# Kernel optimization log

Hardware: AMD Instinct MI355X
Metric: run time of the kernel (lower is better)

The kernel has to match this reference:

```python
import jax, jax.numpy as jnp
import numpy as np

NEG_SLOPE = 0.15


def _gcn_norm(edge_index, num_nodes):
    # PyG GCNConv default: add self-loops, symmetric normalization.
    src = jnp.concatenate([edge_index[0], jnp.arange(num_nodes)])
    dst = jnp.concatenate([edge_index[1], jnp.arange(num_nodes)])
    deg = jax.ops.segment_sum(jnp.ones_like(src, dtype=jnp.float32), dst,
                              num_segments=num_nodes)
    dis = jnp.where(deg > 0, jax.lax.rsqrt(jnp.maximum(deg, 1.0)), 0.0)
    norm = dis[src] * dis[dst]  # [E + N]
    return src, dst, norm


def _gcn_conv(h, W, b, src, dst, norm, num_nodes):
    h = h @ W                                   # dense transform first (PyG order)
    msg = h[src] * norm[:, None]                # gather + scale per edge
    out = jax.ops.segment_sum(msg, dst, num_segments=num_nodes)  # scatter-add
    return out + b


def setup_inputs() -> dict:
    key = jax.random.key(0)
    ks = jax.random.split(key, 16)
    N, E, D = 20000, 320000, 128
    x = jax.random.normal(ks[0], (N, D), dtype=jnp.float32)
    edge_index = jax.random.randint(ks[1], (2, E), 0, N, dtype=jnp.int32)
    edge_attr = jax.random.normal(ks[2], (E, 2), dtype=jnp.float32)

    def lin(k, fi, fo):
        kw, kb = jax.random.split(k)
        s = 1.0 / np.sqrt(fi)
        return (jax.random.uniform(kw, (fi, fo), jnp.float32, -s, s),
                jax.random.uniform(kb, (fo,), jnp.float32, -s, s))

    W1, b1 = lin(ks[3], D, 512)
    W2, b2 = lin(ks[4], 512, 256)
    W3, b3 = lin(ks[5], 256, 128)
    Wp, bp = lin(ks[6], 128, 16)   # pre_fc (128 -> 16)
    Wf1, bf1 = lin(ks[7], 16, 32)  # fallback MLP classifier
    Wf2, bf2 = lin(ks[8], 32, 2)
    return {"x": x, "edge_index": edge_index, "edge_attr": edge_attr,
            "W1": W1, "b1": b1, "W2": W2, "b2": b2, "W3": W3, "b3": b3,
            "Wp": Wp, "bp": bp, "Wf1": Wf1, "bf1": bf1, "Wf2": Wf2, "bf2": bf2}


def reference(x, edge_index, edge_attr, W1, b1, W2, b2, W3, b3,
              Wp, bp, Wf1, bf1, Wf2, bf2):
    N = x.shape[0]
    src, dst, norm = _gcn_norm(edge_index, N)
    lrelu = lambda h: jax.nn.leaky_relu(h, NEG_SLOPE)
    h = lrelu(_gcn_conv(x, W1, b1, src, dst, norm, N))   # dropout = identity (eval)
    h = lrelu(_gcn_conv(h, W2, b2, src, dst, norm, N))
    h = lrelu(_gcn_conv(h, W3, b3, src, dst, norm, N))
    h = h @ Wp + bp                                      # pre_fc: 128 -> 16
    h = lrelu(h @ Wf1 + bf1)                             # classifier MLP
    return h @ Wf2 + bf2                                 # [N, 2]
```

## Files before the change

### kernel.cpp

```cpp
#include <hip/hip_runtime.h>
#include <hip/hip_bf16.h>

typedef __hip_bfloat16 bf16;
typedef unsigned short ushort_t;
typedef __attribute__((ext_vector_type(8))) short short8v;
typedef __attribute__((ext_vector_type(4))) float floatx4;

#define NEG_SLOPE 0.15f

__device__ __forceinline__ float us2f(unsigned short u) {
    unsigned int x = ((unsigned int)u) << 16;
    float f;
    __builtin_memcpy(&f, &x, 4);
    return f;
}
__device__ __forceinline__ unsigned short f2us(float v) {
    bf16 h = __float2bfloat16(v);
    unsigned short u;
    __builtin_memcpy(&u, &h, 2);
    return u;
}

__device__ __forceinline__ int block_flag(const unsigned int* __restrict__ xw) {
    __shared__ int cnt;
    if (threadIdx.x == 0) cnt = 0;
    __syncthreads();
    if (threadIdx.x < 256) {
        unsigned int w = xw[threadIdx.x];
        unsigned int e = (w >> 7) & 0xFF;
        if ((w & 0xFFFF) == 0 || (e >= 100 && e <= 140)) atomicAdd(&cnt, 1);
    }
    __syncthreads();
    return cnt >= 150;
}

__global__ void convert_x_kernel(const void* __restrict__ in, ushort_t* __restrict__ out,
                                 int n) {
    int f = block_flag((const unsigned int*)in);
    int i = blockIdx.x * blockDim.x + threadIdx.x;
    if (i >= n) return;
    out[i] = f ? ((const unsigned short*)in)[i] : f2us(((const float*)in)[i]);
}

struct PrepDesc {
    const void* src[12];
    void* dst[12];
    int n[12];
    int K[12], Nn[12];
};

__global__ void prep_small_kernel(PrepDesc d, const void* __restrict__ xsrc) {
    int f = block_flag((const unsigned int*)xsrc);
    int t = blockIdx.y;
    int i = blockIdx.x * blockDim.x + threadIdx.x;
    if (i >= d.n[t]) return;
    if (d.K[t] == 0) {
        ((float*)d.dst[t])[i] = f ? us2f(((const unsigned short*)d.src[t])[i])
                                  : ((const float*)d.src[t])[i];
    } else {
        int K = d.K[t], Nn = d.Nn[t];
        int n = i / K, k = i - n * K;
        size_t si = (size_t)k * Nn + n;
        ((ushort_t*)d.dst[t])[i] = f ? ((const unsigned short*)d.src[t])[si]
                                     : f2us(((const float*)d.src[t])[si]);
    }
}

__global__ void count_deg_kernel(const int* __restrict__ dst, int* __restrict__ deg,
                                 int E, int N) {
    int i = blockIdx.x * blockDim.x + threadIdx.x;
    if (i < E) {
        int d = dst[i];
        d = d < 0 ? 0 : (d >= N ? N - 1 : d);
        atomicAdd(&deg[d], 1);
    }
}

__global__ void scanA_kernel(const int* __restrict__ deg, int* __restrict__ incl,
                             int* __restrict__ bsum, int N) {
    __shared__ int sh[1024];
    int tid = threadIdx.x;
    int i = blockIdx.x * 1024 + tid;
    int v = (i < N) ? (deg[i] + 1) : 0;
    sh[tid] = v;
    __syncthreads();
    for (int off = 1; off < 1024; off <<= 1) {
        int t = (tid >= off) ? sh[tid - off] : 0;
        __syncthreads();
        sh[tid] += t;
        __syncthreads();
    }
    if (i < N) incl[i] = sh[tid];
    if (tid == 1023) bsum[blockIdx.x] = sh[1023];
}

__global__ void scanC_kernel(const int* __restrict__ deg, const int* __restrict__ incl,
                             const int* __restrict__ bsum, int* __restrict__ offsets,
                             int* __restrict__ cursor, float* __restrict__ dis, int N) {
    __shared__ int base_s;
    if (threadIdx.x == 0) {
        int a = 0;
        for (int b = 0; b < (int)blockIdx.x; ++b) a += bsum[b];
        base_s = a;
    }
    __syncthreads();
    int i = blockIdx.x * 1024 + threadIdx.x;
    if (i >= N) return;
    int base = base_s;
    int d = deg[i] + 1;
    int inc = incl[i];
    int excl = base + inc - d;
    offsets[i] = excl;
    cursor[i] = excl;
    dis[i] = rsqrtf((float)d);
    if (i == N - 1) offsets[N] = base + inc;
}

__global__ void fill_csr_kernel(const int* __restrict__ src, const int* __restrict__ dst,
                                const float* __restrict__ dis, int* __restrict__ cursor,
                                int2* __restrict__ edges, int E, int N, int Etot) {
    int i = blockIdx.x * blockDim.x + threadIdx.x;
    int s, d;
    if (i < E) { s = src[i]; d = dst[i]; }
    else if (i < Etot) { s = d = i - E; }
    else return;
    s = s < 0 ? 0 : (s >= N ? N - 1 : s);
    d = d < 0 ? 0 : (d >= N ? N - 1 : d);
    int pos = atomicAdd(&cursor[d], 1);
    if (pos >= 0 && pos < Etot) edges[pos] = make_int2(s, __float_as_int(dis[s]));
}

template <int VEC> struct LdT;
template <> struct LdT<2> { typedef unsigned int T; };
template <> struct LdT<4> { typedef uint2 T; };

template <int VEC>
__device__ __forceinline__ void addv(typename LdT<VEC>::T u, float w, float* acc);
template <>
__device__ __forceinline__ void addv<2>(unsigned int u, float w, float* acc) {
    acc[0] += w * us2f((unsigned short)(u & 0xFFFF));
    acc[1] += w * us2f((unsigned short)(u >> 16));
}
template <>
__device__ __forceinline__ void addv<4>(uint2 u, float w, float* acc) {
    acc[0] += w * us2f((unsigned short)(u.x & 0xFFFF));
    acc[1] += w * us2f((unsigned short)(u.x >> 16));
    acc[2] += w * us2f((unsigned short)(u.y & 0xFFFF));
    acc[3] += w * us2f((unsigned short)(u.y >> 16));
}

template <int VEC>
__device__ __forceinline__ void agg_core(
    const ushort_t* __restrict__ Hin, const int* __restrict__ offsets,
    const int2* __restrict__ edges, const float* __restrict__ dis,
    int node, int lane, int N, int Etot,
    const float* __restrict__ bias, int do_lrelu, float* outv) {
    typedef typename LdT<VEC>::T LT;
    const int F = VEC * 64;
    int beg = offsets[node], end = offsets[node + 1];
    beg = beg < 0 ? 0 : (beg > Etot ? Etot : beg);
    end = end < beg ? beg : (end > Etot ? Etot : end);

    float acc[VEC];
#pragma unroll
    for (int v = 0; v < VEC; ++v) acc[v] = 0.f;

    int fo = lane * VEC;
    int e = beg;
    for (; e + 8 <= end; e += 8) {
        int2 r[8];
#pragma unroll
        for (int j = 0; j < 8; ++j) r[j] = edges[e + j];
        LT u[8];
#pragma unroll
        for (int j = 0; j < 8; ++j) {
            int s = r[j].x;
            s = s < 0 ? 0 : (s >= N ? N - 1 : s);
            u[j] = *(const LT*)(Hin + (size_t)s * F + fo);
        }
#pragma unroll
        for (int j = 0; j < 8; ++j) addv<VEC>(u[j], __int_as_float(r[j].y), acc);
    }
    if (e + 4 <= end) {
        int2 r[4];
#pragma unroll
        for (int j = 0; j < 4; ++j) r[j] = edges[e + j];
        LT u[4];
#pragma unroll
        for (int j = 0; j < 4; ++j) {
            int s = r[j].x;
            s = s < 0 ? 0 : (s >= N ? N - 1 : s);
            u[j] = *(const LT*)(Hin + (size_t)s * F + fo);
        }
#pragma unroll
        for (int j = 0; j < 4; ++j) addv<VEC>(u[j], __int_as_float(r[j].y), acc);
        e += 4;
    }
    for (; e < end; ++e) {
        int2 r = edges[e];
        int s = r.x;
        s = s < 0 ? 0 : (s >= N ? N - 1 : s);
        LT u = *(const LT*)(Hin + (size_t)s * F + fo);
        addv<VEC>(u, __int_as_float(r.y), acc);
    }

    float dn = dis[node];
#pragma unroll
    for (int v = 0; v < VEC; ++v) {
        float a = acc[v] * dn;
        if (bias) a += bias[fo + v];
        if (do_lrelu) a = (a > 0.f) ? a : a * NEG_SLOPE;
        outv[v] = a;
    }
}

template <int VEC>
__global__ __launch_bounds__(256) void agg_kernel(
    const ushort_t* __restrict__ Hin, ushort_t* __restrict__ OutB,
    const int* __restrict__ offsets, const int2* __restrict__ edges,
    const float* __restrict__ dis, int N, int Etot,
    const float* __restrict__ bias, int do_lrelu) {
    int lane = threadIdx.x & 63;
    int node = blockIdx.x * 4 + (threadIdx.x >> 6);
    if (node >= N) return;
    float outv[VEC];
    agg_core<VEC>(Hin, offsets, edges, dis, node, lane, N, Etot, bias, do_lrelu, outv);
    size_t base = (size_t)node * (VEC * 64) + lane * VEC;
    if (VEC == 2) {
        unsigned int w = ((unsigned int)f2us(outv[1]) << 16) | f2us(outv[0]);
        *(unsigned int*)(OutB + base) = w;
    } else {
        uint2 w;
        w.x = ((unsigned int)f2us(outv[1]) << 16) | f2us(outv[0]);
        w.y = ((unsigned int)f2us(outv[3]) << 16) | f2us(outv[2]);
        *(uint2*)(OutB + base) = w;
    }
}

__global__ __launch_bounds__(256) void agg_head_kernel(
    const ushort_t* __restrict__ Hin,
    const int* __restrict__ offsets, const int2* __restrict__ edges,
    const float* __restrict__ dis, int N, int Etot,
    const float* __restrict__ b3,
    const float* __restrict__ Wp, const float* __restrict__ bp,
    const float* __restrict__ Wf1, const float* __restrict__ bf1v,
    const float* __restrict__ Wf2, const float* __restrict__ bf2v,
    void* __restrict__ out, const void* __restrict__ xsrc) {
    int flag = block_flag((const unsigned int*)xsrc);
    int lane = threadIdx.x & 63;
    int node = blockIdx.x * 4 + (threadIdx.x >> 6);
    if (node >= N) return;
    float h[2];
    agg_core<2>(Hin, offsets, edges, dis, node, lane, N, Etot, b3, 1, h);

    int fo = lane * 2;
    float p[16];
#pragma unroll
    for (int j = 0; j < 16; ++j)
        p[j] = h[0] * Wp[fo * 16 + j] + h[1] * Wp[(fo + 1) * 16 + j];
#pragma unroll
    for (int m = 1; m < 64; m <<= 1) {
#pragma unroll
        for (int j = 0; j < 16; ++j) p[j] += __shfl_xor(p[j], m, 64);
    }
    float a0 = 0.f, a1 = 0.f;
    if (lane < 32) {
        float s = bf1v[lane];
#pragma unroll
        for (int k = 0; k < 16; ++k) s += (p[k] + bp[k]) * Wf1[k * 32 + lane];
        s = (s > 0.f) ? s : s * NEG_SLOPE;
        a0 = s * Wf2[lane * 2 + 0];
        a1 = s * Wf2[lane * 2 + 1];
    }
#pragma unroll
    for (int m = 1; m < 64; m <<= 1) {
        a0 += __shfl_xor(a0, m, 64);
        a1 += __shfl_xor(a1, m, 64);
    }
    if (lane == 0) {
        float o0 = a0 + bf2v[0];
        float o1 = a1 + bf2v[1];
        if (flag) {
            unsigned int w = ((unsigned int)f2us(o1) << 16) | f2us(o0);
            *(unsigned int*)((ushort_t*)out + (size_t)node * 2) = w;
        } else {
            float2 w = make_float2(o0, o1);
            *(float2*)((float*)out + (size_t)node * 2) = w;
        }
    }
}

__global__ __launch_bounds__(256) void mfma_gemm128_kernel(
    const ushort_t* __restrict__ A, const ushort_t* __restrict__ Bt,
    ushort_t* __restrict__ C,
    int M, int K, int Nn, const float* __restrict__ bias, int do_lrelu) {
    __shared__ ushort_t As[128 * 40];
    __shared__ ushort_t Bs[128 * 40];

    int tid = threadIdx.x;
    int row0 = blockIdx.y * 128;
    int col0 = blockIdx.x * 128;
    int lane = tid & 63;
    int w = tid >> 6;
    int quad = lane >> 4;
    int col = lane & 15;
    int wr = (w >> 1) * 64;
    int wc = (w & 1) * 64;

    floatx4 acc[4][4];
#pragma unroll
    for (int i = 0; i < 4; ++i)
#pragma unroll
        for (int j = 0; j < 4; ++j) acc[i][j] = (floatx4){0.f, 0.f, 0.f, 0.f};

    int arow = tid >> 1;
    int aseg = (tid & 1) * 16;

    for (int k0 = 0; k0 < K; k0 += 32) {
        {
            uint4 h0 = {0, 0, 0, 0}, h1 = {0, 0, 0, 0};
            if (row0 + arow < M) {
                size_t g = (size_t)(row0 + arow) * K + k0 + aseg;
                h0 = *(const uint4*)(A + g);
                h1 = *(const uint4*)(A + g + 8);
            }
            int lb = arow * 40 + aseg;
            *(uint4*)&As[lb] = h0;
            *(uint4*)&As[lb + 8] = h1;
        }
        {
            size_t g = (size_t)(col0 + arow) * K + k0 + aseg;
            uint4 b0 = *(const uint4*)(Bt + g);
            uint4 b1 = *(const uint4*)(Bt + g + 8);
            int lb = arow * 40 + aseg;
            *(uint4*)&Bs[lb] = b0;
            *(uint4*)&Bs[lb + 8] = b1;
        }
        __syncthreads();

        short8v af[4], bf[4];
#pragma unroll
        for (int rt = 0; rt < 4; ++rt)
            af[rt] = *(const short8v*)&As[(wr + rt * 16 + col) * 40 + quad * 8];
#pragma unroll
        for (int ct = 0; ct < 4; ++ct)
            bf[ct] = *(const short8v*)&Bs[(wc + ct * 16 + col) * 40 + quad * 8];
#pragma unroll
        for (int rt = 0; rt < 4; ++rt)
#pragma unroll
            for (int ct = 0; ct < 4; ++ct)
                acc[rt][ct] = __builtin_amdgcn_mfma_f32_16x16x32_bf16(
                    af[rt], bf[ct], acc[rt][ct], 0, 0, 0);
        __syncthreads();
    }

#pragma unroll
    for (int rt = 0; rt < 4; ++rt) {
#pragma unroll
        for (int ct = 0; ct < 4; ++ct) {
            int gcol = col0 + wc + ct * 16 + col;
            float bv = bias ? bias[gcol] : 0.f;
#pragma unroll
            for (int r = 0; r < 4; ++r) {
                int grow = row0 + wr + rt * 16 + quad * 4 + r;
                if (grow >= M) continue;
                float v = acc[rt][ct][r] + bv;
                if (do_lrelu) v = (v > 0.f) ? v : v * NEG_SLOPE;
                C[(size_t)grow * Nn + gcol] = f2us(v);
            }
        }
    }
}

__global__ __launch_bounds__(256) void mfma_gemm64_kernel(
    const ushort_t* __restrict__ A, const ushort_t* __restrict__ Bt,
    ushort_t* __restrict__ C,
    int M, int K, int Nn, const float* __restrict__ bias, int do_lrelu) {
    __shared__ ushort_t As[128 * 40];
    __shared__ ushort_t Bs[64 * 40];

    int tid = threadIdx.x;
    int row0 = blockIdx.y * 128;
    int col0 = blockIdx.x * 64;
    int lane = tid & 63;
    int w = tid >> 6;
    int quad = lane >> 4;
    int col = lane & 15;
    int wr = (w >> 1) * 64;
    int wc = (w & 1) * 32;

    floatx4 acc[4][2];
#pragma unroll
    for (int i = 0; i < 4; ++i)
#pragma unroll
        for (int j = 0; j < 2; ++j) acc[i][j] = (floatx4){0.f, 0.f, 0.f, 0.f};

    int arow = tid >> 1;
    int aseg = (tid & 1) * 16;
    int bcol = tid >> 2;
    int bseg = (tid & 3) * 8;

    for (int k0 = 0; k0 < K; k0 += 32) {
        {
            uint4 h0 = {0, 0, 0, 0}, h1 = {0, 0, 0, 0};
            if (row0 + arow < M) {
                size_t g = (size_t)(row0 + arow) * K + k0 + aseg;
                h0 = *(const uint4*)(A + g);
                h1 = *(const uint4*)(A + g + 8);
            }
            int lb = arow * 40 + aseg;
            *(uint4*)&As[lb] = h0;
            *(uint4*)&As[lb + 8] = h1;
        }
        {
            size_t g = (size_t)(col0 + bcol) * K + k0 + bseg;
            *(uint4*)&Bs[bcol * 40 + bseg] = *(const uint4*)(Bt + g);
        }
        __syncthreads();

        short8v af[4], bf[2];
#pragma unroll
        for (int rt = 0; rt < 4; ++rt)
            af[rt] = *(const short8v*)&As[(wr + rt * 16 + col) * 40 + quad * 8];
#pragma unroll
        for (int ct = 0; ct < 2; ++ct)
            bf[ct] = *(const short8v*)&Bs[(wc + ct * 16 + col) * 40 + quad * 8];
#pragma unroll
        for (int rt = 0; rt < 4; ++rt)
#pragma unroll
            for (int ct = 0; ct < 2; ++ct)
                acc[rt][ct] = __builtin_amdgcn_mfma_f32_16x16x32_bf16(
                    af[rt], bf[ct], acc[rt][ct], 0, 0, 0);
        __syncthreads();
    }

#pragma unroll
    for (int rt = 0; rt < 4; ++rt) {
#pragma unroll
        for (int ct = 0; ct < 2; ++ct) {
            int gcol = col0 + wc + ct * 16 + col;
            float bv = bias ? bias[gcol] : 0.f;
#pragma unroll
            for (int r = 0; r < 4; ++r) {
                int grow = row0 + wr + rt * 16 + quad * 4 + r;
                if (grow >= M) continue;
                float v = acc[rt][ct][r] + bv;
                if (do_lrelu) v = (v > 0.f) ? v : v * NEG_SLOPE;
                C[(size_t)grow * Nn + gcol] = f2us(v);
            }
        }
    }
}

extern "C" void kernel_launch(void* const* d_in, const int* in_sizes, int n_in,
                              void* d_out, int out_size, void* d_ws, size_t ws_size,
                              hipStream_t stream) {
    const int* ei = (const int*)d_in[1];

    const int N = in_sizes[0] / 128;
    const int E = in_sizes[1] / 2;
    const int Etot = E + N;
    const int nb = (N + 1023) / 1024;
    const int* srcv = ei;
    const int* dstv = ei + E;

    uintptr_t p = (uintptr_t)d_ws;
    auto alloc = [&](size_t bytes) -> void* {
        p = (p + 255) & ~(uintptr_t)255;
        void* r = (void*)p;
        p += bytes;
        return r;
    };
    ushort_t* xb      = (ushort_t*)alloc((size_t)N * 128 * 2);
    int*      deg     = (int*)alloc((size_t)N * 4);
    int*      offsets = (int*)alloc((size_t)(N + 1) * 4);
    int*      cursor  = (int*)alloc((size_t)N * 4);
    float*    dis     = (float*)alloc((size_t)N * 4);
    int*      incl    = (int*)alloc((size_t)N * 4);
    int*      bsum    = (int*)alloc((size_t)(nb + 1) * 4);
    int2*     edges   = (int2*)alloc((size_t)Etot * 8);

    const int K1 = 128, N1 = 512, K2 = 512, N2 = 256, K3 = 256, N3 = 128;
    ushort_t* W1t = (ushort_t*)alloc((size_t)K1 * N1 * 2);
    ushort_t* W2t = (ushort_t*)alloc((size_t)K2 * N2 * 2);
    ushort_t* W3t = (ushort_t*)alloc((size_t)K3 * N3 * 2);

    float* smalls[9];
    const int wmap[9] = {4, 6, 8, 9, 10, 11, 12, 13, 14};
    for (int t = 0; t < 9; ++t)
        smalls[t] = (float*)alloc((size_t)in_sizes[wmap[t]] * 4);
    const float *b1 = smalls[0], *b2 = smalls[1], *b3 = smalls[2];
    const float *Wp = smalls[3], *bp = smalls[4];
    const float *Wf1 = smalls[5], *bf1v = smalls[6];
    const float *Wf2 = smalls[7], *bf2v = smalls[8];

    ushort_t* BufT0 = (ushort_t*)alloc((size_t)N * 128 * 2);
    ushort_t* BufH1 = (ushort_t*)alloc((size_t)N * 512 * 2);
    ushort_t* BufT2 = (ushort_t*)alloc((size_t)N * 256 * 2);
    ushort_t* t0 = BufT0;
    ushort_t* t3 = BufT0;
    ushort_t* H1 = BufH1;
    ushort_t* H2 = BufH1;
    ushort_t* t2 = BufT2;

    convert_x_kernel<<<(N * 128 + 255) / 256, 256, 0, stream>>>(d_in[0], xb, N * 128);
    {
        PrepDesc pd;
        for (int t = 0; t < 9; ++t) {
            pd.src[t] = d_in[wmap[t]];
            pd.dst[t] = smalls[t];
            pd.n[t] = in_sizes[wmap[t]];
            pd.K[t] = 0; pd.Nn[t] = 0;
        }
        pd.src[9]  = d_in[3]; pd.dst[9]  = W1t; pd.n[9]  = K1 * N1; pd.K[9]  = K1; pd.Nn[9]  = N1;
        pd.src[10] = d_in[5]; pd.dst[10] = W2t; pd.n[10] = K2 * N2; pd.K[10] = K2; pd.Nn[10] = N2;
        pd.src[11] = d_in[7]; pd.dst[11] = W3t; pd.n[11] = K3 * N3; pd.K[11] = K3; pd.Nn[11] = N3;
        dim3 g((K2 * N2 + 255) / 256, 12);
        prep_small_kernel<<<g, 256, 0, stream>>>(pd, d_in[0]);
    }

    hipMemsetAsync(deg, 0, (size_t)N * 4, stream);
    count_deg_kernel<<<(E + 255) / 256, 256, 0, stream>>>(dstv, deg, E, N);
    scanA_kernel<<<nb, 1024, 0, stream>>>(deg, incl, bsum, N);
    scanC_kernel<<<nb, 1024, 0, stream>>>(deg, incl, bsum, offsets, cursor, dis, N);
    fill_csr_kernel<<<(Etot + 255) / 256, 256, 0, stream>>>(srcv, dstv, dis, cursor,
                                                            edges, E, N, Etot);

    int aggGrid = (N + 3) / 4;
    agg_kernel<2><<<aggGrid, 256, 0, stream>>>(xb, t0, offsets, edges, dis,
                                               N, Etot, nullptr, 0);
    {
        dim3 g(N1 / 128, (N + 127) / 128);
        mfma_gemm128_kernel<<<g, 256, 0, stream>>>(t0, W1t, H1, N, K1, N1, b1, 1);
    }
    {
        dim3 g(N2 / 128, (N + 127) / 128);
        mfma_gemm128_kernel<<<g, 256, 0, stream>>>(H1, W2t, t2, N, K2, N2, nullptr, 0);
    }
    agg_kernel<4><<<aggGrid, 256, 0, stream>>>(t2, H2, offsets, edges, dis,
                                               N, Etot, b2, 1);
    {
        dim3 g(N3 / 64, (N + 127) / 128);
        mfma_gemm64_kernel<<<g, 256, 0, stream>>>(H2, W3t, t3, N, K3, N3, nullptr, 0);
    }
    agg_head_kernel<<<aggGrid, 256, 0, stream>>>(t3, offsets, edges, dis, N, Etot,
                                                 b3, Wp, bp, Wf1, bf1v, Wf2, bf2v,
                                                 d_out, d_in[0]);
}
```

Baseline: 277.5 us.

## Fuse x conversion into first aggregation, merge scan kernels, split wide aggregation

Removes the separate x-to-bf16 conversion kernel: the first aggregation now gathers directly from the raw input, in fp32 or bf16. The two-pass degree scan becomes a single kernel in which each block publishes its sum and spins on the sums of earlier blocks, using flags in a buffer that is zeroed along with the degrees. The 256-wide aggregation now uses a second grid dimension with 2 features per lane instead of 4. This saves launches and an extra pass over x, at the cost of fp32 gathers at twice the bytes per lane, a decoupled-lookback scan that depends on earlier blocks being scheduled, and duplicated edge-list reads across the feature halves.

```diff
diff --git a/kernel.cpp b/kernel.cpp
--- a/kernel.cpp
+++ b/kernel.cpp
@@ -32,14 +32,6 @@
     }
     __syncthreads();
     return cnt >= 150;
-}
-
-__global__ void convert_x_kernel(const void* __restrict__ in, ushort_t* __restrict__ out,
-                                 int n) {
-    int f = block_flag((const unsigned int*)in);
-    int i = blockIdx.x * blockDim.x + threadIdx.x;
-    if (i >= n) return;
-    out[i] = f ? ((const unsigned short*)in)[i] : f2us(((const float*)in)[i]);
 }
 
 struct PrepDesc {
@@ -76,11 +68,14 @@
     }
 }
 
-__global__ void scanA_kernel(const int* __restrict__ deg, int* __restrict__ incl,
-                             int* __restrict__ bsum, int N) {
+__global__ void scan_merged_kernel(const int* __restrict__ deg, int* __restrict__ offsets,
+                                   int* __restrict__ cursor, float* __restrict__ dis,
+                                   int* __restrict__ bsumf, int N) {
     __shared__ int sh[1024];
+    __shared__ int base_s;
     int tid = threadIdx.x;
-    int i = blockIdx.x * 1024 + tid;
+    int b = blockIdx.x;
+    int i = b * 1024 + tid;
     int v = (i < N) ? (deg[i] + 1) : 0;
     sh[tid] = v;
     __syncthreads();
@@ -90,30 +85,31 @@
         sh[tid] += t;
         __syncthreads();
     }
-    if (i < N) incl[i] = sh[tid];
-    if (tid == 1023) bsum[blockIdx.x] = sh[1023];
-}
-
-__global__ void scanC_kernel(const int* __restrict__ deg, const int* __restrict__ incl,
-                             const int* __restrict__ bsum, int* __restrict__ offsets,
-                             int* __restrict__ cursor, float* __restrict__ dis, int N) {
-    __shared__ int base_s;
-    if (threadIdx.x == 0) {
+    if (tid == 0) {
+        __hip_atomic_store(&bsumf[b], sh[1023] + 1, __ATOMIC_RELEASE,
+                           __HIP_MEMORY_SCOPE_AGENT);
         int a = 0;
-        for (int b = 0; b < (int)blockIdx.x; ++b) a += bsum[b];
+        for (int pb = 0; pb < b; ++pb) {
+            int val;
+            do {
+                val = __hip_atomic_load(&bsumf[pb], __ATOMIC_ACQUIRE,
+                                        __HIP_MEMORY_SCOPE_AGENT);
+            } while (val == 0);
+            a += val - 1;
+        }
         base_s = a;
     }
     __syncthreads();
-    int i = blockIdx.x * 1024 + threadIdx.x;
-    if (i >= N) return;
-    int base = base_s;
-    int d = deg[i] + 1;
-    int inc = incl[i];
-    int excl = base + inc - d;
-    offsets[i] = excl;
-    cursor[i] = excl;
-    dis[i] = rsqrtf((float)d);
-    if (i == N - 1) offsets[N] = base + inc;
+    if (i < N) {
+        int base = base_s;
+        int d = deg[i] + 1;
+        int inc = sh[tid];
+        int excl = base + inc - d;
+        offsets[i] = excl;
+        cursor[i] = excl;
+        dis[i] = rsqrtf((float)d);
+        if (i == N - 1) offsets[N] = base + inc;
+    }
 }
 
 __global__ void fill_csr_kernel(const int* __restrict__ src, const int* __restrict__ dst,
@@ -130,111 +126,115 @@
     if (pos >= 0 && pos < Etot) edges[pos] = make_int2(s, __float_as_int(dis[s]));
 }
 
-template <int VEC> struct LdT;
-template <> struct LdT<2> { typedef unsigned int T; };
-template <> struct LdT<4> { typedef uint2 T; };
-
-template <int VEC>
-__device__ __forceinline__ void addv(typename LdT<VEC>::T u, float w, float* acc);
-template <>
-__device__ __forceinline__ void addv<2>(unsigned int u, float w, float* acc) {
-    acc[0] += w * us2f((unsigned short)(u & 0xFFFF));
-    acc[1] += w * us2f((unsigned short)(u >> 16));
-}
-template <>
-__device__ __forceinline__ void addv<4>(uint2 u, float w, float* acc) {
-    acc[0] += w * us2f((unsigned short)(u.x & 0xFFFF));
-    acc[1] += w * us2f((unsigned short)(u.x >> 16));
-    acc[2] += w * us2f((unsigned short)(u.y & 0xFFFF));
-    acc[3] += w * us2f((unsigned short)(u.y >> 16));
-}
-
-template <int VEC>
-__device__ __forceinline__ void agg_core(
-    const ushort_t* __restrict__ Hin, const int* __restrict__ offsets,
-    const int2* __restrict__ edges, const float* __restrict__ dis,
-    int node, int lane, int N, int Etot,
-    const float* __restrict__ bias, int do_lrelu, float* outv) {
-    typedef typename LdT<VEC>::T LT;
-    const int F = VEC * 64;
-    int beg = offsets[node], end = offsets[node + 1];
-    beg = beg < 0 ? 0 : (beg > Etot ? Etot : beg);
-    end = end < beg ? beg : (end > Etot ? Etot : end);
-
-    float acc[VEC];
-#pragma unroll
-    for (int v = 0; v < VEC; ++v) acc[v] = 0.f;
-
-    int fo = lane * VEC;
+__device__ __forceinline__ void gather2(
+    const ushort_t* __restrict__ Hin, int F, int fo,
+    const int2* __restrict__ edges, int beg, int end, int N,
+    float& a0, float& a1) {
+    a0 = 0.f; a1 = 0.f;
     int e = beg;
     for (; e + 8 <= end; e += 8) {
         int2 r[8];
 #pragma unroll
         for (int j = 0; j < 8; ++j) r[j] = edges[e + j];
-        LT u[8];
+        unsigned int u[8];
 #pragma unroll
         for (int j = 0; j < 8; ++j) {
             int s = r[j].x;
             s = s < 0 ? 0 : (s >= N ? N - 1 : s);
-            u[j] = *(const LT*)(Hin + (size_t)s * F + fo);
-        }
-#pragma unroll
-        for (int j = 0; j < 8; ++j) addv<VEC>(u[j], __int_as_float(r[j].y), acc);
-    }
-    if (e + 4 <= end) {
-        int2 r[4];
-#pragma unroll
-        for (int j = 0; j < 4; ++j) r[j] = edges[e + j];
-        LT u[4];
-#pragma unroll
-        for (int j = 0; j < 4; ++j) {
-            int s = r[j].x;
-            s = s < 0 ? 0 : (s >= N ? N - 1 : s);
-            u[j] = *(const LT*)(Hin + (size_t)s * F + fo);
-        }
-#pragma unroll
-        for (int j = 0; j < 4; ++j) addv<VEC>(u[j], __int_as_float(r[j].y), acc);
-        e += 4;
+            u[j] = *(const unsigned int*)(Hin + (size_t)s * F + fo);
+        }
+#pragma unroll
+        for (int j = 0; j < 8; ++j) {
+            float w = __int_as_float(r[j].y);
+            a0 += w * us2f((unsigned short)(u[j] & 0xFFFF));
+            a1 += w * us2f((unsigned short)(u[j] >> 16));
+        }
     }
     for (; e < end; ++e) {
         int2 r = edges[e];
         int s = r.x;
         s = s < 0 ? 0 : (s >= N ? N - 1 : s);
-        LT u = *(const LT*)(Hin + (size_t)s * F + fo);
-        addv<VEC>(u, __int_as_float(r.y), acc);
-    }
-
-    float dn = dis[node];
-#pragma unroll
-    for (int v = 0; v < VEC; ++v) {
-        float a = acc[v] * dn;
-        if (bias) a += bias[fo + v];
-        if (do_lrelu) a = (a > 0.f) ? a : a * NEG_SLOPE;
-        outv[v] = a;
-    }
-}
-
-template <int VEC>
+        unsigned int u = *(const unsigned int*)(Hin + (size_t)s * F + fo);
+        float w = __int_as_float(r.y);
+        a0 += w * us2f((unsigned short)(u & 0xFFFF));
+        a1 += w * us2f((unsigned short)(u >> 16));
+    }
+}
+
 __global__ __launch_bounds__(256) void agg_kernel(
     const ushort_t* __restrict__ Hin, ushort_t* __restrict__ OutB,
     const int* __restrict__ offsets, const int2* __restrict__ edges,
-    const float* __restrict__ dis, int N, int Etot,
+    const float* __restrict__ dis, int N, int Etot, int F,
     const float* __restrict__ bias, int do_lrelu) {
     int lane = threadIdx.x & 63;
     int node = blockIdx.x * 4 + (threadIdx.x >> 6);
     if (node >= N) return;
-    float outv[VEC];
-    agg_core<VEC>(Hin, offsets, edges, dis, node, lane, N, Etot, bias, do_lrelu, outv);
-    size_t base = (size_t)node * (VEC * 64) + lane * VEC;
-    if (VEC == 2) {
-        unsigned int w = ((unsigned int)f2us(outv[1]) << 16) | f2us(outv[0]);
-        *(unsigned int*)(OutB + base) = w;
+    int fo = blockIdx.y * 128 + lane * 2;
+    int beg = offsets[node], end = offsets[node + 1];
+    beg = beg < 0 ? 0 : (beg > Etot ? Etot : beg);
+    end = end < beg ? beg : (end > Etot ? Etot : end);
+    float a0, a1;
+    gather2(Hin, F, fo, edges, beg, end, N, a0, a1);
+    float dn = dis[node];
+    a0 *= dn; a1 *= dn;
+    if (bias) { a0 += bias[fo]; a1 += bias[fo + 1]; }
+    if (do_lrelu) {
+        a0 = (a0 > 0.f) ? a0 : a0 * NEG_SLOPE;
+        a1 = (a1 > 0.f) ? a1 : a1 * NEG_SLOPE;
+    }
+    unsigned int w = ((unsigned int)f2us(a1) << 16) | f2us(a0);
+    *(unsigned int*)(OutB + (size_t)node * F + fo) = w;
+}
+
+__global__ __launch_bounds__(256) void agg_x_kernel(
+    const void* __restrict__ X, ushort_t* __restrict__ OutB,
+    const int* __restrict__ offsets, const int2* __restrict__ edges,
+    const float* __restrict__ dis, int N, int Etot) {
+    int flag = block_flag((const unsigned int*)X);
+    int lane = threadIdx.x & 63;
+    int node = blockIdx.x * 4 + (threadIdx.x >> 6);
+    if (node >= N) return;
+    int beg = offsets[node], end = offsets[node + 1];
+    beg = beg < 0 ? 0 : (beg > Etot ? Etot : beg);
+    end = end < beg ? beg : (end > Etot ? Etot : end);
+    float a0 = 0.f, a1 = 0.f;
+    if (flag) {
+        gather2((const ushort_t*)X, 128, lane * 2, edges, beg, end, N, a0, a1);
     } else {
-        uint2 w;
-        w.x = ((unsigned int)f2us(outv[1]) << 16) | f2us(outv[0]);
-        w.y = ((unsigned int)f2us(outv[3]) << 16) | f2us(outv[2]);
-        *(uint2*)(OutB + base) = w;
-    }
+        const float2* Xf = (const float2*)X;
+        int e = beg;
+        for (; e + 4 <= end; e += 4) {
+            int2 r[4];
+#pragma unroll
+            for (int j = 0; j < 4; ++j) r[j] = edges[e + j];
+            float2 u[4];
+#pragma unroll
+            for (int j = 0; j < 4; ++j) {
+                int s = r[j].x;
+                s = s < 0 ? 0 : (s >= N ? N - 1 : s);
+                u[j] = Xf[(size_t)s * 64 + lane];
+            }
+#pragma unroll
+            for (int j = 0; j < 4; ++j) {
+                float w = __int_as_float(r[j].y);
+                a0 += w * u[j].x;
+                a1 += w * u[j].y;
+            }
+        }
+        for (; e < end; ++e) {
+            int2 r = edges[e];
+            int s = r.x;
+            s = s < 0 ? 0 : (s >= N ? N - 1 : s);
+            float2 u = Xf[(size_t)s * 64 + lane];
+            float w = __int_as_float(r.y);
+            a0 += w * u.x;
+            a1 += w * u.y;
+        }
+    }
+    float dn = dis[node];
+    a0 *= dn; a1 *= dn;
+    unsigned int w = ((unsigned int)f2us(a1) << 16) | f2us(a0);
+    *(unsigned int*)(OutB + (size_t)node * 128 + lane * 2) = w;
 }
 
 __global__ __launch_bounds__(256) void agg_head_kernel(
@@ -250,14 +250,22 @@
     int lane = threadIdx.x & 63;
     int node = blockIdx.x * 4 + (threadIdx.x >> 6);
     if (node >= N) return;
-    float h[2];
-    agg_core<2>(Hin, offsets, edges, dis, node, lane, N, Etot, b3, 1, h);
-
     int fo = lane * 2;
+    int beg = offsets[node], end = offsets[node + 1];
+    beg = beg < 0 ? 0 : (beg > Etot ? Etot : beg);
+    end = end < beg ? beg : (end > Etot ? Etot : end);
+    float h0, h1;
+    gather2(Hin, 128, fo, edges, beg, end, N, h0, h1);
+    float dn = dis[node];
+    h0 = h0 * dn + b3[fo];
+    h1 = h1 * dn + b3[fo + 1];
+    h0 = (h0 > 0.f) ? h0 : h0 * NEG_SLOPE;
+    h1 = (h1 > 0.f) ? h1 : h1 * NEG_SLOPE;
+
     float p[16];
 #pragma unroll
     for (int j = 0; j < 16; ++j)
-        p[j] = h[0] * Wp[fo * 16 + j] + h[1] * Wp[(fo + 1) * 16 + j];
+        p[j] = h0 * Wp[fo * 16 + j] + h1 * Wp[(fo + 1) * 16 + j];
 #pragma unroll
     for (int m = 1; m < 64; m <<= 1) {
 #pragma unroll
@@ -284,8 +292,7 @@
             unsigned int w = ((unsigned int)f2us(o1) << 16) | f2us(o0);
             *(unsigned int*)((ushort_t*)out + (size_t)node * 2) = w;
         } else {
-            float2 w = make_float2(o0, o1);
-            *(float2*)((float*)out + (size_t)node * 2) = w;
+            *(float2*)((float*)out + (size_t)node * 2) = make_float2(o0, o1);
         }
     }
 }
@@ -471,13 +478,11 @@
         p += bytes;
         return r;
     };
-    ushort_t* xb      = (ushort_t*)alloc((size_t)N * 128 * 2);
-    int*      deg     = (int*)alloc((size_t)N * 4);
+    int*      deg     = (int*)alloc((size_t)(N + nb + 1) * 4);
+    int*      bsumf   = deg + N;
     int*      offsets = (int*)alloc((size_t)(N + 1) * 4);
     int*      cursor  = (int*)alloc((size_t)N * 4);
     float*    dis     = (float*)alloc((size_t)N * 4);
-    int*      incl    = (int*)alloc((size_t)N * 4);
-    int*      bsum    = (int*)alloc((size_t)(nb + 1) * 4);
     int2*     edges   = (int2*)alloc((size_t)Etot * 8);
 
     const int K1 = 128, N1 = 512, K2 = 512, N2 = 256, K3 = 256, N3 = 128;
@@ -503,7 +508,6 @@
     ushort_t* H2 = BufH1;
     ushort_t* t2 = BufT2;
 
-    convert_x_kernel<<<(N * 128 + 255) / 256, 256, 0, stream>>>(d_in[0], xb, N * 128);
     {
         PrepDesc pd;
         for (int t = 0; t < 9; ++t) {
@@ -519,16 +523,14 @@
         prep_small_kernel<<<g, 256, 0, stream>>>(pd, d_in[0]);
     }
 
-    hipMemsetAsync(deg, 0, (size_t)N * 4, stream);
+    hipMemsetAsync(deg, 0, (size_t)(N + nb + 1) * 4, stream);
     count_deg_kernel<<<(E + 255) / 256, 256, 0, stream>>>(dstv, deg, E, N);
-    scanA_kernel<<<nb, 1024, 0, stream>>>(deg, incl, bsum, N);
-    scanC_kernel<<<nb, 1024, 0, stream>>>(deg, incl, bsum, offsets, cursor, dis, N);
+    scan_merged_kernel<<<nb, 1024, 0, stream>>>(deg, offsets, cursor, dis, bsumf, N);
     fill_csr_kernel<<<(Etot + 255) / 256, 256, 0, stream>>>(srcv, dstv, dis, cursor,
                                                             edges, E, N, Etot);
 
     int aggGrid = (N + 3) / 4;
-    agg_kernel<2><<<aggGrid, 256, 0, stream>>>(xb, t0, offsets, edges, dis,
-                                               N, Etot, nullptr, 0);
+    agg_x_kernel<<<aggGrid, 256, 0, stream>>>(d_in[0], t0, offsets, edges, dis, N, Etot);
     {
         dim3 g(N1 / 128, (N + 127) / 128);
         mfma_gemm128_kernel<<<g, 256, 0, stream>>>(t0, W1t, H1, N, K1, N1, b1, 1);
@@ -537,8 +539,10 @@
         dim3 g(N2 / 128, (N + 127) / 128);
         mfma_gemm128_kernel<<<g, 256, 0, stream>>>(H1, W2t, t2, N, K2, N2, nullptr, 0);
     }
-    agg_kernel<4><<<aggGrid, 256, 0, stream>>>(t2, H2, offsets, edges, dis,
-                                               N, Etot, b2, 1);
+    {
+        dim3 g(aggGrid, N2 / 128);
+        agg_kernel<<<g, 256, 0, stream>>>(t2, H2, offsets, edges, dis, N, Etot, N2, b2, 1);
+    }
     {
         dim3 g(N3 / 64, (N + 127) / 128);
         mfma_gemm64_kernel<<<g, 256, 0, stream>>>(H2, W3t, t3, N, K3, N3, nullptr, 0);
```

Result: slower. 289.5 us (+4.3%).

## Fuse CSR build into one grid-barrier kernel and fold x conversion into prep

Applied to the files above, without the earlier changes.

Merges degree count, block scan, offset computation and CSR fill into a single persistent kernel synchronised by an atomic grid barrier. The x-to-bf16 conversion and zeroing of the degree/barrier counters move into the batched prep kernel, which removes a memset and several launches. All GEMMs now use the 128x64 tile variant, which gives smaller tiles and more blocks for layers 1 and 2. The grid barrier relies on all nb (~20) blocks of 1024 threads being co-resident, and the count and fill phases now run on far fewer threads using grid-stride loops.

```diff
diff --git a/kernel.cpp b/kernel.cpp
--- a/kernel.cpp
+++ b/kernel.cpp
@@ -34,31 +34,35 @@
     return cnt >= 150;
 }
 
-__global__ void convert_x_kernel(const void* __restrict__ in, ushort_t* __restrict__ out,
-                                 int n) {
-    int f = block_flag((const unsigned int*)in);
-    int i = blockIdx.x * blockDim.x + threadIdx.x;
-    if (i >= n) return;
-    out[i] = f ? ((const unsigned short*)in)[i] : f2us(((const float*)in)[i]);
-}
-
 struct PrepDesc {
-    const void* src[12];
-    void* dst[12];
-    int n[12];
-    int K[12], Nn[12];
+    const void* src[14];
+    void* dst[14];
+    int n[14];
+    int K[14], Nn[14];
 };
 
 __global__ void prep_small_kernel(PrepDesc d, const void* __restrict__ xsrc) {
     int f = block_flag((const unsigned int*)xsrc);
     int t = blockIdx.y;
+    int Kt = d.K[t];
+    int nt = d.n[t];
+    if (Kt == -2) {
+        ushort_t* out = (ushort_t*)d.dst[t];
+        const void* in = d.src[t];
+        int stride = gridDim.x * blockDim.x;
+        for (int i = blockIdx.x * blockDim.x + threadIdx.x; i < nt; i += stride)
+            out[i] = f ? ((const unsigned short*)in)[i] : f2us(((const float*)in)[i]);
+        return;
+    }
     int i = blockIdx.x * blockDim.x + threadIdx.x;
-    if (i >= d.n[t]) return;
-    if (d.K[t] == 0) {
+    if (i >= nt) return;
+    if (Kt == -1) {
+        ((int*)d.dst[t])[i] = 0;
+    } else if (Kt == 0) {
         ((float*)d.dst[t])[i] = f ? us2f(((const unsigned short*)d.src[t])[i])
                                   : ((const float*)d.src[t])[i];
     } else {
-        int K = d.K[t], Nn = d.Nn[t];
+        int K = Kt, Nn = d.Nn[t];
         int n = i / K, k = i - n * K;
         size_t si = (size_t)k * Nn + n;
         ((ushort_t*)d.dst[t])[i] = f ? ((const unsigned short*)d.src[t])[si]
@@ -66,22 +70,37 @@
     }
 }
 
-__global__ void count_deg_kernel(const int* __restrict__ dst, int* __restrict__ deg,
-                                 int E, int N) {
-    int i = blockIdx.x * blockDim.x + threadIdx.x;
-    if (i < E) {
+__device__ __forceinline__ void gbar(int* bar, int target) {
+    __syncthreads();
+    if (threadIdx.x == 0) {
+        __hip_atomic_fetch_add(bar, 1, __ATOMIC_ACQ_REL, __HIP_MEMORY_SCOPE_AGENT);
+        while (__hip_atomic_load(bar, __ATOMIC_ACQUIRE, __HIP_MEMORY_SCOPE_AGENT)
+               < target) {}
+    }
+    __syncthreads();
+}
+
+__global__ __launch_bounds__(1024) void csr_mega_kernel(
+    const int* __restrict__ src, const int* __restrict__ dst,
+    int* __restrict__ deg, int* __restrict__ bar,
+    int* __restrict__ offsets, int* __restrict__ cursor, float* __restrict__ dis,
+    int* __restrict__ bsum, int2* __restrict__ edges,
+    int E, int N, int Etot, int nb) {
+    __shared__ int sh[1024];
+    __shared__ int base_s;
+    int tid = threadIdx.x;
+    int b = blockIdx.x;
+    int gtid = b * 1024 + tid;
+    int gsz = nb * 1024;
+
+    for (int i = gtid; i < E; i += gsz) {
         int d = dst[i];
         d = d < 0 ? 0 : (d >= N ? N - 1 : d);
         atomicAdd(&deg[d], 1);
     }
-}
-
-__global__ void scanA_kernel(const int* __restrict__ deg, int* __restrict__ incl,
-                             int* __restrict__ bsum, int N) {
-    __shared__ int sh[1024];
-    int tid = threadIdx.x;
-    int i = blockIdx.x * 1024 + tid;
-    int v = (i < N) ? (deg[i] + 1) : 0;
+    gbar(bar, nb);
+
+    int v = (gtid < N) ? (deg[gtid] + 1) : 0;
     sh[tid] = v;
     __syncthreads();
     for (int off = 1; off < 1024; off <<= 1) {
@@ -90,44 +109,35 @@
         sh[tid] += t;
         __syncthreads();
     }
-    if (i < N) incl[i] = sh[tid];
-    if (tid == 1023) bsum[blockIdx.x] = sh[1023];
-}
-
-__global__ void scanC_kernel(const int* __restrict__ deg, const int* __restrict__ incl,
-                             const int* __restrict__ bsum, int* __restrict__ offsets,
-                             int* __restrict__ cursor, float* __restrict__ dis, int N) {
-    __shared__ int base_s;
-    if (threadIdx.x == 0) {
+    int inc = sh[tid];
+    if (tid == 1023) bsum[b] = sh[1023];
+    gbar(bar, 2 * nb);
+
+    if (tid == 0) {
         int a = 0;
-        for (int b = 0; b < (int)blockIdx.x; ++b) a += bsum[b];
+        for (int pb = 0; pb < b; ++pb) a += bsum[pb];
         base_s = a;
     }
     __syncthreads();
-    int i = blockIdx.x * 1024 + threadIdx.x;
-    if (i >= N) return;
-    int base = base_s;
-    int d = deg[i] + 1;
-    int inc = incl[i];
-    int excl = base + inc - d;
-    offsets[i] = excl;
-    cursor[i] = excl;
-    dis[i] = rsqrtf((float)d);
-    if (i == N - 1) offsets[N] = base + inc;
-}
-
-__global__ void fill_csr_kernel(const int* __restrict__ src, const int* __restrict__ dst,
-                                const float* __restrict__ dis, int* __restrict__ cursor,
-                                int2* __restrict__ edges, int E, int N, int Etot) {
-    int i = blockIdx.x * blockDim.x + threadIdx.x;
-    int s, d;
-    if (i < E) { s = src[i]; d = dst[i]; }
-    else if (i < Etot) { s = d = i - E; }
-    else return;
-    s = s < 0 ? 0 : (s >= N ? N - 1 : s);
-    d = d < 0 ? 0 : (d >= N ? N - 1 : d);
-    int pos = atomicAdd(&cursor[d], 1);
-    if (pos >= 0 && pos < Etot) edges[pos] = make_int2(s, __float_as_int(dis[s]));
+    if (gtid < N) {
+        int base = base_s;
+        int excl = base + inc - v;
+        offsets[gtid] = excl;
+        cursor[gtid] = excl;
+        dis[gtid] = rsqrtf((float)v);
+        if (gtid == N - 1) offsets[N] = base + inc;
+    }
+    gbar(bar, 3 * nb);
+
+    for (int i = gtid; i < Etot; i += gsz) {
+        int s, d;
+        if (i < E) { s = src[i]; d = dst[i]; }
+        else { s = d = i - E; }
+        s = s < 0 ? 0 : (s >= N ? N - 1 : s);
+        d = d < 0 ? 0 : (d >= N ? N - 1 : d);
+        int pos = atomicAdd(&cursor[d], 1);
+        if (pos >= 0 && pos < Etot) edges[pos] = make_int2(s, __float_as_int(dis[s]));
+    }
 }
 
 template <int VEC> struct LdT;
@@ -284,37 +294,38 @@
             unsigned int w = ((unsigned int)f2us(o1) << 16) | f2us(o0);
             *(unsigned int*)((ushort_t*)out + (size_t)node * 2) = w;
         } else {
-            float2 w = make_float2(o0, o1);
-            *(float2*)((float*)out + (size_t)node * 2) = w;
-        }
-    }
-}
-
-__global__ __launch_bounds__(256) void mfma_gemm128_kernel(
+            *(float2*)((float*)out + (size_t)node * 2) = make_float2(o0, o1);
+        }
+    }
+}
+
+__global__ __launch_bounds__(256) void mfma_gemm_kernel(
     const ushort_t* __restrict__ A, const ushort_t* __restrict__ Bt,
     ushort_t* __restrict__ C,
     int M, int K, int Nn, const float* __restrict__ bias, int do_lrelu) {
     __shared__ ushort_t As[128 * 40];
-    __shared__ ushort_t Bs[128 * 40];
+    __shared__ ushort_t Bs[64 * 40];
 
     int tid = threadIdx.x;
     int row0 = blockIdx.y * 128;
-    int col0 = blockIdx.x * 128;
+    int col0 = blockIdx.x * 64;
     int lane = tid & 63;
     int w = tid >> 6;
     int quad = lane >> 4;
     int col = lane & 15;
     int wr = (w >> 1) * 64;
-    int wc = (w & 1) * 64;
-
-    floatx4 acc[4][4];
+    int wc = (w & 1) * 32;
+
+    floatx4 acc[4][2];
 #pragma unroll
     for (int i = 0; i < 4; ++i)
 #pragma unroll
-        for (int j = 0; j < 4; ++j) acc[i][j] = (floatx4){0.f, 0.f, 0.f, 0.f};
+        for (int j = 0; j < 2; ++j) acc[i][j] = (floatx4){0.f, 0.f, 0.f, 0.f};
 
     int arow = tid >> 1;
     int aseg = (tid & 1) * 16;
+    int bcol = tid >> 2;
+    int bseg = (tid & 3) * 8;
 
     for (int k0 = 0; k0 < K; k0 += 32) {
         {
@@ -329,26 +340,22 @@
             *(uint4*)&As[lb + 8] = h1;
         }
         {
-            size_t g = (size_t)(col0 + arow) * K + k0 + aseg;
-            uint4 b0 = *(const uint4*)(Bt + g);
-            uint4 b1 = *(const uint4*)(Bt + g + 8);
-            int lb = arow * 40 + aseg;
-            *(uint4*)&Bs[lb] = b0;
-            *(uint4*)&Bs[lb + 8] = b1;
+            size_t g = (size_t)(col0 + bcol) * K + k0 + bseg;
+            *(uint4*)&Bs[bcol * 40 + bseg] = *(const uint4*)(Bt + g);
         }
         __syncthreads();
 
-        short8v af[4], bf[4];
+        short8v af[4], bf[2];
 #pragma unroll
         for (int rt = 0; rt < 4; ++rt)
             af[rt] = *(const short8v*)&As[(wr + rt * 16 + col) * 40 + quad * 8];
 #pragma unroll
-        for (int ct = 0; ct < 4; ++ct)
+        for (int ct = 0; ct < 2; ++ct)
             bf[ct] = *(const short8v*)&Bs[(wc + ct * 16 + col) * 40 + quad * 8];
 #pragma unroll
         for (int rt = 0; rt < 4; ++rt)
 #pragma unroll
-            for (int ct = 0; ct < 4; ++ct)
+            for (int ct = 0; ct < 2; ++ct)
                 acc[rt][ct] = __builtin_amdgcn_mfma_f32_16x16x32_bf16(
                     af[rt], bf[ct], acc[rt][ct], 0, 0, 0);
         __syncthreads();
@@ -357,7 +364,7 @@
 #pragma unroll
     for (int rt = 0; rt < 4; ++rt) {
 #pragma unroll
-        for (int ct = 0; ct < 4; ++ct) {
+        for (int ct = 0; ct < 2; ++ct) {
             int gcol = col0 + wc + ct * 16 + col;
             float bv = bias ? bias[gcol] : 0.f;
 #pragma unroll
@@ -372,86 +379,6 @@
     }
 }
 
-__global__ __launch_bounds__(256) void mfma_gemm64_kernel(
-    const ushort_t* __restrict__ A, const ushort_t* __restrict__ Bt,
-    ushort_t* __restrict__ C,
-    int M, int K, int Nn, const float* __restrict__ bias, int do_lrelu) {
-    __shared__ ushort_t As[128 * 40];
-    __shared__ ushort_t Bs[64 * 40];
-
-    int tid = threadIdx.x;
-    int row0 = blockIdx.y * 128;
-    int col0 = blockIdx.x * 64;
-    int lane = tid & 63;
-    int w = tid >> 6;
-    int quad = lane >> 4;
-    int col = lane & 15;
-    int wr = (w >> 1) * 64;
-    int wc = (w & 1) * 32;
-
-    floatx4 acc[4][2];
-#pragma unroll
-    for (int i = 0; i < 4; ++i)
-#pragma unroll
-        for (int j = 0; j < 2; ++j) acc[i][j] = (floatx4){0.f, 0.f, 0.f, 0.f};
-
-    int arow = tid >> 1;
-    int aseg = (tid & 1) * 16;
-    int bcol = tid >> 2;
-    int bseg = (tid & 3) * 8;
-
-    for (int k0 = 0; k0 < K; k0 += 32) {
-        {
-            uint4 h0 = {0, 0, 0, 0}, h1 = {0, 0, 0, 0};
-            if (row0 + arow < M) {
-                size_t g = (size_t)(row0 + arow) * K + k0 + aseg;
-                h0 = *(const uint4*)(A + g);
-                h1 = *(const uint4*)(A + g + 8);
-            }
-            int lb = arow * 40 + aseg;
-            *(uint4*)&As[lb] = h0;
-            *(uint4*)&As[lb + 8] = h1;
-        }
-        {
-            size_t g = (size_t)(col0 + bcol) * K + k0 + bseg;
-            *(uint4*)&Bs[bcol * 40 + bseg] = *(const uint4*)(Bt + g);
-        }
-        __syncthreads();
-
-        short8v af[4], bf[2];
-#pragma unroll
-        for (int rt = 0; rt < 4; ++rt)
-            af[rt] = *(const short8v*)&As[(wr + rt * 16 + col) * 40 + quad * 8];
-#pragma unroll
-        for (int ct = 0; ct < 2; ++ct)
-            bf[ct] = *(const short8v*)&Bs[(wc + ct * 16 + col) * 40 + quad * 8];
-#pragma unroll
-        for (int rt = 0; rt < 4; ++rt)
-#pragma unroll
-            for (int ct = 0; ct < 2; ++ct)
-                acc[rt][ct] = __builtin_amdgcn_mfma_f32_16x16x32_bf16(
-                    af[rt], bf[ct], acc[rt][ct], 0, 0, 0);
-        __syncthreads();
-    }
-
-#pragma unroll
-    for (int rt = 0; rt < 4; ++rt) {
-#pragma unroll
-        for (int ct = 0; ct < 2; ++ct) {
-            int gcol = col0 + wc + ct * 16 + col;
-            float bv = bias ? bias[gcol] : 0.f;
-#pragma unroll
-            for (int r = 0; r < 4; ++r) {
-                int grow = row0 + wr + rt * 16 + quad * 4 + r;
-                if (grow >= M) continue;
-                float v = acc[rt][ct][r] + bv;
-                if (do_lrelu) v = (v > 0.f) ? v : v * NEG_SLOPE;
-                C[(size_t)grow * Nn + gcol] = f2us(v);
-            }
-        }
-    }
-}
-
 extern "C" void kernel_launch(void* const* d_in, const int* in_sizes, int n_in,
                               void* d_out, int out_size, void* d_ws, size_t ws_size,
                               hipStream_t stream) {
@@ -471,14 +398,14 @@
         p += bytes;
         return r;
     };
-    ushort_t* xb      = (ushort_t*)alloc((size_t)N * 128 * 2);
-    int*      deg     = (int*)alloc((size_t)N * 4);
+    int*      deg     = (int*)alloc((size_t)(N + 4) * 4);
+    int*      bar     = deg + N;
     int*      offsets = (int*)alloc((size_t)(N + 1) * 4);
     int*      cursor  = (int*)alloc((size_t)N * 4);
     float*    dis     = (float*)alloc((size_t)N * 4);
-    int*      incl    = (int*)alloc((size_t)N * 4);
     int*      bsum    = (int*)alloc((size_t)(nb + 1) * 4);
     int2*     edges   = (int2*)alloc((size_t)Etot * 8);
+    ushort_t* xb      = (ushort_t*)alloc((size_t)N * 128 * 2);
 
     const int K1 = 128, N1 = 512, K2 = 512, N2 = 256, K3 = 256, N3 = 128;
     ushort_t* W1t = (ushort_t*)alloc((size_t)K1 * N1 * 2);
@@ -503,7 +430,6 @@
     ushort_t* H2 = BufH1;
     ushort_t* t2 = BufT2;
 
-    convert_x_kernel<<<(N * 128 + 255) / 256, 256, 0, stream>>>(d_in[0], xb, N * 128);
     {
         PrepDesc pd;
         for (int t = 0; t < 9; ++t) {
@@ -515,33 +441,31 @@
         pd.src[9]  = d_in[3]; pd.dst[9]  = W1t; pd.n[9]  = K1 * N1; pd.K[9]  = K1; pd.Nn[9]  = N1;
         pd.src[10] = d_in[5]; pd.dst[10] = W2t; pd.n[10] = K2 * N2; pd.K[10] = K2; pd.Nn[10] = N2;
         pd.src[11] = d_in[7]; pd.dst[11] = W3t; pd.n[11] = K3 * N3; pd.K[11] = K3; pd.Nn[11] = N3;
-        dim3 g((K2 * N2 + 255) / 256, 12);
+        pd.src[12] = nullptr; pd.dst[12] = deg; pd.n[12] = N + 4; pd.K[12] = -1; pd.Nn[12] = 0;
+        pd.src[13] = d_in[0]; pd.dst[13] = xb;  pd.n[13] = N * 128; pd.K[13] = -2; pd.Nn[13] = 0;
+        dim3 g((K2 * N2 + 255) / 256, 14);
         prep_small_kernel<<<g, 256, 0, stream>>>(pd, d_in[0]);
     }
 
-    hipMemsetAsync(deg, 0, (size_t)N * 4, stream);
-    count_deg_kernel<<<(E + 255) / 256, 256, 0, stream>>>(dstv, deg, E, N);
-    scanA_kernel<<<nb, 1024, 0, stream>>>(deg, incl, bsum, N);
-    scanC_kernel<<<nb, 1024, 0, stream>>>(deg, incl, bsum, offsets, cursor, dis, N);
-    fill_csr_kernel<<<(Etot + 255) / 256, 256, 0, stream>>>(srcv, dstv, dis, cursor,
-                                                            edges, E, N, Etot);
+    csr_mega_kernel<<<nb, 1024, 0, stream>>>(srcv, dstv, deg, bar, offsets, cursor,
+                                             dis, bsum, edges, E, N, Etot, nb);
 
     int aggGrid = (N + 3) / 4;
     agg_kernel<2><<<aggGrid, 256, 0, stream>>>(xb, t0, offsets, edges, dis,
                                                N, Etot, nullptr, 0);
     {
-        dim3 g(N1 / 128, (N + 127) / 128);
-        mfma_gemm128_kernel<<<g, 256, 0, stream>>>(t0, W1t, H1, N, K1, N1, b1, 1);
+        dim3 g(N1 / 64, (N + 127) / 128);
+        mfma_gemm_kernel<<<g, 256, 0, stream>>>(t0, W1t, H1, N, K1, N1, b1, 1);
     }
     {
-        dim3 g(N2 / 128, (N + 127) / 128);
-        mfma_gemm128_kernel<<<g, 256, 0, stream>>>(H1, W2t, t2, N, K2, N2, nullptr, 0);
+        dim3 g(N2 / 64, (N + 127) / 128);
+        mfma_gemm_kernel<<<g, 256, 0, stream>>>(H1, W2t, t2, N, K2, N2, nullptr, 0);
     }
     agg_kernel<4><<<aggGrid, 256, 0, stream>>>(t2, H2, offsets, edges, dis,
                                                N, Etot, b2, 1);
     {
         dim3 g(N3 / 64, (N + 127) / 128);
-        mfma_gemm64_kernel<<<g, 256, 0, stream>>>(H2, W3t, t3, N, K3, N3, nullptr, 0);
+        mfma_gemm_kernel<<<g, 256, 0, stream>>>(H2, W3t, t3, N, K3, N3, nullptr, 0);
     }
     agg_head_kernel<<<aggGrid, 256, 0, stream>>>(t3, offsets, edges, dis, N, Etot,
                                                  b3, Wp, bp, Wf1, bf1v, Wf2, bf2v,
```

Measured after the change: 333.1 us. 1.2x slower.
